# Optimization experiments

Measured on AMD Instinct MI355X. Metric: run time of the kernel, lower is better.

## Reference

```python
import jax, jax.numpy as jnp
import numpy as np
from jax import lax

B, C, H, W, K, R = 8, 64, 128, 128, 3, 4  # batch, channels, height, width, kernel_size, region_number


def _leaky(x):
    return jnp.where(x >= 0, x, 0.1 * x)


def _asign_index(kernel, guide):
    # kernel: (b,R,c,h,w), guide: (b,R,h,w) -> hard top-1 region routing -> (b,c,h,w)
    mask = jax.nn.one_hot(jnp.argmax(guide, axis=1), R, axis=1, dtype=kernel.dtype)  # (b,R,h,w)
    return jnp.sum(kernel * mask[:, :, None], axis=1)


def _conv2d(x, w, pad):
    return lax.conv_general_dilated(x, w, (1, 1), [(pad, pad), (pad, pad)],
                                    dimension_numbers=('NCHW', 'OIHW', 'NCHW'))


def setup_inputs() -> dict:
    key = jax.random.key(0)
    ks = jax.random.split(key, 12)
    s = 0.05
    return {
        'x0': jax.random.normal(ks[0], (B, C, H, W), jnp.float32),
        'deg': jax.random.normal(ks[1], (B, C), jnp.float32),
        'q_map': jax.random.normal(ks[2], (B, 1, H, W), jnp.float32),
        'w_k1': jax.random.normal(ks[3], (C, C), jnp.float32) * s,
        'w_k2': jax.random.normal(ks[4], (R, C * K * K, C // R), jnp.float32) * s,
        'w_conv': jax.random.normal(ks[5], (C, C), jnp.float32) * s,
        'b_conv': jax.random.normal(ks[6], (C,), jnp.float32) * s,
        'w_ca1': jax.random.normal(ks[7], (C, C), jnp.float32) * s,
        'w_ca2': jax.random.normal(ks[8], (R, C, C // R), jnp.float32) * s,
        'w_g1': jax.random.normal(ks[9], (R, 1, K, K), jnp.float32) * s,
        'b_g1': jnp.zeros((R,), jnp.float32),
        'w_g2': jax.random.normal(ks[10], (R, 1, K, K), jnp.float32) * s,
        'b_g2': jnp.zeros((R,), jnp.float32),
    }


def reference(x0, deg, q_map, w_k1, w_k2, w_conv, b_conv, w_ca1, w_ca2, w_g1, b_g1, w_g2, b_g2):
    b, c, h, w = x0.shape
    pad = (K - 1) // 2
    # --- dynamic per-sample, per-channel depthwise kernels from degradation rep ---
    y = _leaky(deg @ w_k1.T)                                             # 1x1 conv1d -> (b, c)
    kflat = jnp.einsum('bgi,goi->bgo', y.reshape(b, R, c // R), w_k2)    # grouped 1x1 conv1d
    kernel = kflat.reshape(b, R, c, K, K).transpose(0, 2, 1, 3, 4)       # (b,c,R,K,K)
    rhs = kernel.reshape(b * c * R, 1, K, K)
    out = lax.conv_general_dilated(x0.reshape(1, b * c, h, w), rhs, (1, 1),
                                   [(pad, pad), (pad, pad)],
                                   dimension_numbers=('NCHW', 'OIHW', 'NCHW'),
                                   feature_group_count=b * c)            # (1, b*c*R, h, w)
    out = _leaky(out).reshape(b, c, R, h, w).transpose(0, 2, 1, 3, 4)    # (b,R,c,h,w)
    g1 = _conv2d(q_map, w_g1, 1) + b_g1[None, :, None, None]             # (b,R,h,w)
    out = _asign_index(out, g1)                                          # (b,c,h,w)
    out = jnp.einsum('bchw,oc->bohw', out, w_conv) + b_conv[None, :, None, None]
    # --- channel-attention (CA_layer) branch ---
    a = _leaky(deg @ w_ca1.T)                                            # (b, c)
    att = jax.nn.sigmoid(jnp.einsum('bgi,goi->bgo', a.reshape(b, R, c // R), w_ca2))  # (b,R,c)
    out2 = x0[:, None] * att[:, :, :, None, None]                        # (b,R,c,h,w)
    g2 = _conv2d(q_map, w_g2, 1) + b_g2[None, :, None, None]
    out2 = _asign_index(out2, g2)
    return out + out2
```

## Files before the change

### kernel.cpp

```cpp
#include <hip/hip_runtime.h>
#include <hip/hip_bf16.h>
#include <math.h>

#define Bn 8
#define Cn 64
#define Hn 128
#define Wn 128
#define Rn 4

typedef __bf16 v8bf __attribute__((ext_vector_type(8)));
typedef float  v16f __attribute__((ext_vector_type(16)));

__device__ __forceinline__ float leaky(float x) { return x >= 0.f ? x : 0.1f * x; }

__device__ __forceinline__ unsigned bf16pair(float a, float b) {
    __hip_bfloat16 ha = __float2bfloat16(a);
    __hip_bfloat16 hb = __float2bfloat16(b);
    return (unsigned)*reinterpret_cast<unsigned short*>(&ha) |
           ((unsigned)*reinterpret_cast<unsigned short*>(&hb) << 16);
}

__global__ __launch_bounds__(256) void precomp_kernel(
    const float* __restrict__ deg, const float* __restrict__ w_k1,
    const float* __restrict__ w_k2, const float* __restrict__ w_ca1,
    const float* __restrict__ w_ca2, const float* __restrict__ w_conv,
    float* __restrict__ kern_g, float* __restrict__ att_g,
    unsigned short* __restrict__ wbf)
{
    const int tid = threadIdx.x;
    if (blockIdx.x == Bn) {
        for (int f = tid; f < Cn * Cn; f += 256) {
            __hip_bfloat16 hx = __float2bfloat16(w_conv[f]);
            wbf[f] = *reinterpret_cast<unsigned short*>(&hx);
        }
        return;
    }
    const int b = blockIdx.x;
    __shared__ float y_s[64], a_s[64];
    if (tid < 64) {
        float sy = 0.f, sa = 0.f;
#pragma unroll 8
        for (int j = 0; j < 64; ++j) {
            float d = deg[b * 64 + j];
            sy += d * w_k1[tid * 64 + j];
            sa += d * w_ca1[tid * 64 + j];
        }
        y_s[tid] = leaky(sy);
        a_s[tid] = leaky(sa);
    }
    __syncthreads();
    for (int f = tid; f < Cn * Rn * 9; f += 256) {
        int c = f / 36;
        int j = f - c * 36;
        int r = j / 9;
        int kk = j - r * 9;
        int o = c * 9 + kk;
        const float* wp = &w_k2[(r * 576 + o) * 16];
        const float* yp = &y_s[r * 16];
        float s = 0.f;
#pragma unroll
        for (int i = 0; i < 16; ++i) s += yp[i] * wp[i];
        kern_g[b * 2304 + f] = s;
    }
    {
        int r = tid >> 6, o = tid & 63;
        const float* wp = &w_ca2[(r * 64 + o) * 16];
        const float* ap = &a_s[r * 16];
        float s = 0.f;
#pragma unroll
        for (int i = 0; i < 16; ++i) s += ap[i] * wp[i];
        att_g[b * 256 + tid] = 1.f / (1.f + expf(-s));
    }
}

__global__ __launch_bounds__(512) void da_main(
    const float* __restrict__ x0, const float* __restrict__ q_map,
    const unsigned short* __restrict__ wbf, const float* __restrict__ b_conv,
    const float* __restrict__ w_g1, const float* __restrict__ b_g1,
    const float* __restrict__ w_g2, const float* __restrict__ b_g2,
    const float* __restrict__ kern_g, const float* __restrict__ att_g,
    float* __restrict__ out)
{
    __shared__ __align__(16) float kern_lds[Cn * 48];
    __shared__ __align__(16) unsigned short wc_lds[8][Cn][8];
    __shared__ __align__(16) unsigned short t_lds[Wn * Cn];
    __shared__ float att_lds[Rn * 68];
    __shared__ float bias_lds[Cn];
    __shared__ unsigned ridx[Wn];

    const int tid = threadIdx.x;
    const int ob = blockIdx.x;
    const int sb = ((ob & 7) << 7) | (ob >> 3);
    const int b = sb >> 7;
    const int h = sb & 127;

    const int lane = tid & 63;
    const int w = tid & 127;
    const int q = tid >> 7;

    for (int f = tid; f < Cn * Rn * 9; f += 512) {
        int c = f / 36;
        int j = f - c * 36;
        int r = j / 9;
        int kk = j - r * 9;
        kern_lds[c * 48 + r * 12 + kk] = kern_g[b * 2304 + f];
    }
    {
        int cq = tid & 7, o = tid >> 3;
        *(v8bf*)&wc_lds[cq][o][0] = *(const v8bf*)&wbf[o * 64 + cq * 8];
    }
    if (tid < 256) att_lds[(tid >> 6) * 68 + (tid & 63)] = att_g[b * 256 + tid];
    if (tid < 64) bias_lds[tid] = b_conv[tid];

    if (tid < 128) {
        const int wc = tid;
        float qv[9];
#pragma unroll
        for (int dh = 0; dh < 3; ++dh) {
            int row = h - 1 + dh;
#pragma unroll
            for (int dw = 0; dw < 3; ++dw) {
                int col = wc - 1 + dw;
                qv[dh * 3 + dw] = (row >= 0 && row < Hn && col >= 0 && col < Wn)
                                      ? q_map[(b * Hn + row) * Wn + col] : 0.f;
            }
        }
        float best1 = -1e30f, best2 = -1e30f;
        int r1 = 0, r2 = 0;
#pragma unroll
        for (int r = 0; r < Rn; ++r) {
            float s1 = b_g1[r], s2 = b_g2[r];
#pragma unroll
            for (int k = 0; k < 9; ++k) {
                s1 += qv[k] * w_g1[r * 9 + k];
                s2 += qv[k] * w_g2[r * 9 + k];
            }
            if (s1 > best1) { best1 = s1; r1 = r; }
            if (s2 > best2) { best2 = s2; r2 = r; }
        }
        ridx[wc] = (unsigned)r1 | ((unsigned)r2 << 16);
    }
    __syncthreads();

    const bool okm = (h > 0);
    const bool okp = (h < Hn - 1);
    const float* xbase = x0 + (size_t)(b * Cn) * Hn * Wn + h * Wn + w;
    const int swz = (w & 7) << 4;
    const int r1 = (int)(ridx[w] & 0xffffu);
    const int eoff = (lane == 0) ? ((w == 0) ? 0 : -1)
                   : (lane == 63) ? ((w == 127) ? 0 : 1) : 0;
    const bool eok = !((lane == 0 && w == 0) || (lane == 63 && w == 127));

    float nvm[2], nv0[2], nvp[2], nem[2], ne0[2], nep[2];

#define LOADP(P)                                                          \
    do {                                                                  \
        _Pragma("unroll")                                                 \
        for (int u = 0; u < 2; ++u) {                                     \
            const float* xc = xbase + (16 * q + 2 * (P) + u) * (Hn * Wn); \
            nvm[u] = okm ? xc[-Wn] : 0.f;                                 \
            nv0[u] = xc[0];                                               \
            nvp[u] = okp ? xc[Wn] : 0.f;                                  \
            const float* xe = xc + eoff;                                  \
            nem[u] = okm ? xe[-Wn] : 0.f;                                 \
            ne0[u] = xe[0];                                               \
            nep[u] = okp ? xe[Wn] : 0.f;                                  \
        }                                                                 \
    } while (0)

    LOADP(0);
#pragma unroll
    for (int p = 0; p < 8; ++p) {
        float avm[2] = {nvm[0], nvm[1]}, av0[2] = {nv0[0], nv0[1]},
              avp[2] = {nvp[0], nvp[1]};
        float aem[2] = {nem[0], nem[1]}, ae0[2] = {ne0[0], ne0[1]},
              aep[2] = {nep[0], nep[1]};
        if (p < 7) LOADP(p + 1);

        float tt[2];
#pragma unroll
        for (int u = 0; u < 2; ++u) {
            const int c = 16 * q + 2 * p + u;
            float vm = avm[u], v0 = av0[u], vp = avp[u];
            float lm = __shfl_up(vm, 1), l0 = __shfl_up(v0, 1), lp = __shfl_up(vp, 1);
            float rm = __shfl_down(vm, 1), r0 = __shfl_down(v0, 1), rp = __shfl_down(vp, 1);
            float em = eok ? aem[u] : 0.f;
            float e0 = eok ? ae0[u] : 0.f;
            float ep = eok ? aep[u] : 0.f;
            if (lane == 0)  { lm = em; l0 = e0; lp = ep; }
            if (lane == 63) { rm = em; r0 = e0; rp = ep; }
            const float* kp = &kern_lds[c * 48 + r1 * 12];
            float4 k03 = *(const float4*)kp;
            float4 k47 = *(const float4*)(kp + 4);
            float k8 = kp[8];
            float t = lm * k03.x + vm * k03.y + rm * k03.z
                    + l0 * k03.w + v0 * k47.x + r0 * k47.y
                    + lp * k47.z + vp * k47.w + rp * k8;
            tt[u] = leaky(t);
        }
        unsigned pk = bf16pair(tt[0], tt[1]);
        int cbyte = (16 * q + 2 * p) * 2;
        *(unsigned*)((char*)t_lds + w * 128 + (cbyte ^ swz)) = pk;
    }
#undef LOADP
    __syncthreads();

    const int v = tid >> 6;
    const int wt = v & 3;
    const int oh = v >> 2;
    const int col = lane & 31;
    const int kh = lane >> 5;
    const int wn = wt * 32 + col;

    v8bf Bf[4];
#pragma unroll
    for (int ks = 0; ks < 4; ++ks) {
        int cbyte = (16 * ks + 8 * kh) * 2;
        Bf[ks] = *(const v8bf*)((const char*)t_lds + wn * 128 + (cbyte ^ ((wn & 7) << 4)));
    }

    v16f acc;
#pragma unroll
    for (int i = 0; i < 16; ++i) acc[i] = 0.f;

#pragma unroll
    for (int ks = 0; ks < 4; ++ks) {
        const int cq = 2 * ks + kh;
        v8bf Af = *(const v8bf*)&wc_lds[cq][oh * 32 + col][0];
        acc = __builtin_amdgcn_mfma_f32_32x32x16_bf16(Af, Bf[ks], acc, 0, 0, 0);
    }

    const int r2e = (int)(ridx[wn] >> 16);
    const float* xcol = x0 + ((size_t)(b * Cn + oh * 32) * Hn + h) * Wn + wn;
    float* ocol = out + ((size_t)(b * Cn + oh * 32) * Hn + h) * Wn + wn;

#pragma unroll
    for (int r = 0; r < 16; ++r) {
        int row = (r & 3) + 8 * (r >> 2) + 4 * kh;
        int o = oh * 32 + row;
        float xv = xcol[(size_t)row * (Hn * Wn)];
        float res = acc[r] + bias_lds[o] + xv * att_lds[r2e * 68 + o];
        ocol[(size_t)row * (Hn * Wn)] = res;
    }
}

extern "C" void kernel_launch(void* const* d_in, const int* in_sizes, int n_in,
                              void* d_out, int out_size, void* d_ws, size_t ws_size,
                              hipStream_t stream)
{
    const float* x0     = (const float*)d_in[0];
    const float* deg    = (const float*)d_in[1];
    const float* q_map  = (const float*)d_in[2];
    const float* w_k1   = (const float*)d_in[3];
    const float* w_k2   = (const float*)d_in[4];
    const float* w_conv = (const float*)d_in[5];
    const float* b_conv = (const float*)d_in[6];
    const float* w_ca1  = (const float*)d_in[7];
    const float* w_ca2  = (const float*)d_in[8];
    const float* w_g1   = (const float*)d_in[9];
    const float* b_g1   = (const float*)d_in[10];
    const float* w_g2   = (const float*)d_in[11];
    const float* b_g2   = (const float*)d_in[12];
    float* outp   = (float*)d_out;
    float* kern_g = (float*)d_ws;
    float* att_g  = kern_g + Bn * Cn * Rn * 9;
    unsigned short* wbf = (unsigned short*)(att_g + Bn * 256);

    precomp_kernel<<<Bn + 1, 256, 0, stream>>>(deg, w_k1, w_k2, w_ca1, w_ca2,
                                               w_conv, kern_g, att_g, wbf);
    da_main<<<Bn * Hn, 512, 0, stream>>>(x0, q_map, wbf, b_conv,
                                         w_g1, b_g1, w_g2, b_g2,
                                         kern_g, att_g, outp);
}
```

Before: 36.14 us.

## Fuse per-sample kernel/attention precompute into main kernel, drop precomp launch

Removes the separate precompute kernel and has every block of the main kernel recompute the dynamic depthwise kernels, channel-attention weights and bf16 conversion of w_conv directly into shared memory. This eliminates one kernel launch and the global workspace round trip between the two kernels. In exchange each of the 1024 blocks redundantly computes the small matvecs (64x64 and 2304x16 dot products), adding per-block prologue work and an extra barrier before the main loop.

```diff
diff --git a/kernel.cpp b/kernel.cpp
--- a/kernel.cpp
+++ b/kernel.cpp
@@ -20,23 +20,33 @@
            ((unsigned)*reinterpret_cast<unsigned short*>(&hb) << 16);
 }
 
-__global__ __launch_bounds__(256) void precomp_kernel(
+__global__ __launch_bounds__(512) void da_main(
+    const float* __restrict__ x0, const float* __restrict__ q_map,
+    const float* __restrict__ w_conv, const float* __restrict__ b_conv,
+    const float* __restrict__ w_g1, const float* __restrict__ b_g1,
+    const float* __restrict__ w_g2, const float* __restrict__ b_g2,
     const float* __restrict__ deg, const float* __restrict__ w_k1,
     const float* __restrict__ w_k2, const float* __restrict__ w_ca1,
-    const float* __restrict__ w_ca2, const float* __restrict__ w_conv,
-    float* __restrict__ kern_g, float* __restrict__ att_g,
-    unsigned short* __restrict__ wbf)
+    const float* __restrict__ w_ca2, float* __restrict__ out)
 {
+    __shared__ __align__(16) float kern_lds[Cn * 48];
+    __shared__ __align__(16) unsigned short wc_lds[8][Cn][8];
+    __shared__ __align__(16) unsigned short t_lds[Wn * Cn];
+    __shared__ float att_lds[Rn * 68];
+    __shared__ float bias_lds[Cn];
+    __shared__ unsigned ridx[Wn];
+    __shared__ float y_s[64], a_s[64];
+
     const int tid = threadIdx.x;
-    if (blockIdx.x == Bn) {
-        for (int f = tid; f < Cn * Cn; f += 256) {
-            __hip_bfloat16 hx = __float2bfloat16(w_conv[f]);
-            wbf[f] = *reinterpret_cast<unsigned short*>(&hx);
-        }
-        return;
-    }
-    const int b = blockIdx.x;
-    __shared__ float y_s[64], a_s[64];
+    const int ob = blockIdx.x;
+    const int sb = ((ob & 7) << 7) | (ob >> 3);
+    const int b = sb >> 7;
+    const int h = sb & 127;
+
+    const int lane = tid & 63;
+    const int w = tid & 127;
+    const int q = tid >> 7;
+
     if (tid < 64) {
         float sy = 0.f, sa = 0.f;
 #pragma unroll 8
@@ -47,9 +57,51 @@
         }
         y_s[tid] = leaky(sy);
         a_s[tid] = leaky(sa);
+        bias_lds[tid] = b_conv[tid];
+    }
+    {
+        int cq = tid & 7, o = tid >> 3;
+        const float* src = &w_conv[o * 64 + cq * 8];
+        float4 s0 = *(const float4*)src;
+        float4 s1 = *(const float4*)(src + 4);
+        uint4 pkw;
+        pkw.x = bf16pair(s0.x, s0.y);
+        pkw.y = bf16pair(s0.z, s0.w);
+        pkw.z = bf16pair(s1.x, s1.y);
+        pkw.w = bf16pair(s1.z, s1.w);
+        *(uint4*)&wc_lds[cq][o][0] = pkw;
+    }
+    if (tid < 128) {
+        const int wc = tid;
+        float qv[9];
+#pragma unroll
+        for (int dh = 0; dh < 3; ++dh) {
+            int row = h - 1 + dh;
+#pragma unroll
+            for (int dw = 0; dw < 3; ++dw) {
+                int col = wc - 1 + dw;
+                qv[dh * 3 + dw] = (row >= 0 && row < Hn && col >= 0 && col < Wn)
+                                      ? q_map[(b * Hn + row) * Wn + col] : 0.f;
+            }
+        }
+        float best1 = -1e30f, best2 = -1e30f;
+        int r1 = 0, r2 = 0;
+#pragma unroll
+        for (int r = 0; r < Rn; ++r) {
+            float s1 = b_g1[r], s2 = b_g2[r];
+#pragma unroll
+            for (int k = 0; k < 9; ++k) {
+                s1 += qv[k] * w_g1[r * 9 + k];
+                s2 += qv[k] * w_g2[r * 9 + k];
+            }
+            if (s1 > best1) { best1 = s1; r1 = r; }
+            if (s2 > best2) { best2 = s2; r2 = r; }
+        }
+        ridx[wc] = (unsigned)r1 | ((unsigned)r2 << 16);
     }
     __syncthreads();
-    for (int f = tid; f < Cn * Rn * 9; f += 256) {
+
+    for (int f = tid; f < Cn * Rn * 9; f += 512) {
         int c = f / 36;
         int j = f - c * 36;
         int r = j / 9;
@@ -60,85 +112,16 @@
         float s = 0.f;
 #pragma unroll
         for (int i = 0; i < 16; ++i) s += yp[i] * wp[i];
-        kern_g[b * 2304 + f] = s;
-    }
-    {
+        kern_lds[c * 48 + r * 12 + kk] = s;
+    }
+    if (tid < 256) {
         int r = tid >> 6, o = tid & 63;
         const float* wp = &w_ca2[(r * 64 + o) * 16];
         const float* ap = &a_s[r * 16];
         float s = 0.f;
 #pragma unroll
         for (int i = 0; i < 16; ++i) s += ap[i] * wp[i];
-        att_g[b * 256 + tid] = 1.f / (1.f + expf(-s));
-    }
-}
-
-__global__ __launch_bounds__(512) void da_main(
-    const float* __restrict__ x0, const float* __restrict__ q_map,
-    const unsigned short* __restrict__ wbf, const float* __restrict__ b_conv,
-    const float* __restrict__ w_g1, const float* __restrict__ b_g1,
-    const float* __restrict__ w_g2, const float* __restrict__ b_g2,
-    const float* __restrict__ kern_g, const float* __restrict__ att_g,
-    float* __restrict__ out)
-{
-    __shared__ __align__(16) float kern_lds[Cn * 48];
-    __shared__ __align__(16) unsigned short wc_lds[8][Cn][8];
-    __shared__ __align__(16) unsigned short t_lds[Wn * Cn];
-    __shared__ float att_lds[Rn * 68];
-    __shared__ float bias_lds[Cn];
-    __shared__ unsigned ridx[Wn];
-
-    const int tid = threadIdx.x;
-    const int ob = blockIdx.x;
-    const int sb = ((ob & 7) << 7) | (ob >> 3);
-    const int b = sb >> 7;
-    const int h = sb & 127;
-
-    const int lane = tid & 63;
-    const int w = tid & 127;
-    const int q = tid >> 7;
-
-    for (int f = tid; f < Cn * Rn * 9; f += 512) {
-        int c = f / 36;
-        int j = f - c * 36;
-        int r = j / 9;
-        int kk = j - r * 9;
-        kern_lds[c * 48 + r * 12 + kk] = kern_g[b * 2304 + f];
-    }
-    {
-        int cq = tid & 7, o = tid >> 3;
-        *(v8bf*)&wc_lds[cq][o][0] = *(const v8bf*)&wbf[o * 64 + cq * 8];
-    }
-    if (tid < 256) att_lds[(tid >> 6) * 68 + (tid & 63)] = att_g[b * 256 + tid];
-    if (tid < 64) bias_lds[tid] = b_conv[tid];
-
-    if (tid < 128) {
-        const int wc = tid;
-        float qv[9];
-#pragma unroll
-        for (int dh = 0; dh < 3; ++dh) {
-            int row = h - 1 + dh;
-#pragma unroll
-            for (int dw = 0; dw < 3; ++dw) {
-                int col = wc - 1 + dw;
-                qv[dh * 3 + dw] = (row >= 0 && row < Hn && col >= 0 && col < Wn)
-                                      ? q_map[(b * Hn + row) * Wn + col] : 0.f;
-            }
-        }
-        float best1 = -1e30f, best2 = -1e30f;
-        int r1 = 0, r2 = 0;
-#pragma unroll
-        for (int r = 0; r < Rn; ++r) {
-            float s1 = b_g1[r], s2 = b_g2[r];
-#pragma unroll
-            for (int k = 0; k < 9; ++k) {
-                s1 += qv[k] * w_g1[r * 9 + k];
-                s2 += qv[k] * w_g2[r * 9 + k];
-            }
-            if (s1 > best1) { best1 = s1; r1 = r; }
-            if (s2 > best2) { best2 = s2; r2 = r; }
-        }
-        ridx[wc] = (unsigned)r1 | ((unsigned)r2 << 16);
+        att_lds[r * 68 + o] = 1.f / (1.f + expf(-s));
     }
     __syncthreads();
 
@@ -261,14 +244,9 @@
     const float* b_g1   = (const float*)d_in[10];
     const float* w_g2   = (const float*)d_in[11];
     const float* b_g2   = (const float*)d_in[12];
-    float* outp   = (float*)d_out;
-    float* kern_g = (float*)d_ws;
-    float* att_g  = kern_g + Bn * Cn * Rn * 9;
-    unsigned short* wbf = (unsigned short*)(att_g + Bn * 256);
-
-    precomp_kernel<<<Bn + 1, 256, 0, stream>>>(deg, w_k1, w_k2, w_ca1, w_ca2,
-                                               w_conv, kern_g, att_g, wbf);
-    da_main<<<Bn * Hn, 512, 0, stream>>>(x0, q_map, wbf, b_conv,
+    float* outp = (float*)d_out;
+
+    da_main<<<Bn * Hn, 512, 0, stream>>>(x0, q_map, w_conv, b_conv,
                                          w_g1, b_g1, w_g2, b_g2,
-                                         kern_g, att_g, outp);
+                                         deg, w_k1, w_k2, w_ca1, w_ca2, outp);
 }
```

Measured after the change: 39.39 us. 1.09x slower.
